# Kernel tuning notes

Hardware: AMD Instinct MI355X
Metric: run time of the kernel (lower is better)

## Reference

```python
import jax, jax.numpy as jnp
from jax import lax
import numpy as np


def _majority_filter(x, footprint_size, num_bins):
    # x: [B, H, W] float labels in [0, num_bins).
    # Faithful to torch majority_filter: replicate-pad, per-pixel histogram
    # (torch.histc bins=256 over [0,255] == integer-value counts for integer
    # labels; restricting to num_bins bins is exact since labels < num_bins),
    # mode = argmax of counts with ties broken toward the smaller label
    # (torch.argmax and jnp.argmax both return the first maximum).
    p = footprint_size // 2
    xp = jnp.pad(x, ((0, 0), (p, p), (p, p)), mode='edge')  # [B, H+2p, W+2p]
    bins = jnp.arange(num_bins, dtype=xp.dtype)
    onehot = (xp[..., None] == bins).astype(jnp.float32)  # [B, H+2p, W+2p, num_bins]
    counts = lax.reduce_window(
        onehot, jnp.float32(0), lax.add,
        window_dimensions=(1, footprint_size, footprint_size, 1),
        window_strides=(1, 1, 1, 1), padding='VALID')  # [B, H, W, num_bins]
    return jnp.argmax(counts, axis=-1).astype(x.dtype)


def setup_inputs() -> dict:
    key = jax.random.key(0)
    B, H, W = 8, 768, 768
    NUM_LABELS = 8  # cluster_range=(2, 8) -> labels in [0, 8)
    clusters = jax.random.randint(key, (B, H, W), 0, NUM_LABELS).astype(jnp.float32)
    return {"clusters": clusters, "footprint_size": 3, "num_bins": NUM_LABELS, "max_iter": 8}


def reference(clusters, footprint_size, num_bins, max_iter):
    # clean_clusters: iterate the majority filter up to max_iter times,
    # stopping early once the map is unchanged (|old - new| <= 1e-5 everywhere).
    def cond(state):
        t, i, changed = state
        return jnp.logical_and(i < max_iter, changed)

    def body(state):
        t, i, _ = state
        nt = _majority_filter(t, footprint_size, num_bins)
        changed = jnp.any(jnp.abs(t - nt) > 1e-5)
        return (nt, i + 1, changed)

    t, _, _ = lax.while_loop(cond, body, (clusters, jnp.int32(0), jnp.array(True)))
    return t
```

## Files before the change

### kernel.cpp

```cpp
#include <hip/hip_runtime.h>


static constexpr int IMG = 768;
static constexpr int NBX = 16;
static constexpr int NBY = 16;

__device__ __forceinline__ unsigned bfi(unsigned m, unsigned a, unsigned b) {
  unsigned r;
  asm("v_bfi_b32 %0, %1, %2, %3" : "=v"(r) : "v"(m), "v"(a), "v"(b));
  return r;
}
__device__ __forceinline__ unsigned dppUp(unsigned x) {
  return (unsigned)__builtin_amdgcn_update_dpp(0, (int)x, 0x138, 0xF, 0xF, true);
}
__device__ __forceinline__ unsigned dppDn(unsigned x) {
  return (unsigned)__builtin_amdgcn_update_dpp(0, (int)x, 0x130, 0xF, 0xF, true);
}
__device__ __forceinline__ unsigned alignb(unsigned hi, unsigned lo, int s) {
  return __builtin_amdgcn_alignbit(hi, lo, s);
}

struct C4 { unsigned b0, b1, b2, b3; };

__device__ __forceinline__ unsigned gt4(const C4& x, const C4& y) {
  unsigned d = x.b0 ^ y.b0;
  unsigned g = d & x.b0;
  d = x.b1 ^ y.b1; g = bfi(d, x.b1, g);
  d = x.b2 ^ y.b2; g = bfi(d, x.b2, g);
  d = x.b3 ^ y.b3; g = bfi(d, x.b3, g);
  return g;
}
__device__ __forceinline__ C4 sel4(unsigned G, const C4& x, const C4& y) {
  C4 r; r.b0 = bfi(G, x.b0, y.b0); r.b1 = bfi(G, x.b1, y.b1);
  r.b2 = bfi(G, x.b2, y.b2); r.b3 = bfi(G, x.b3, y.b3); return r;
}
__device__ __forceinline__ void tourn8(const C4 c[8],
                                       unsigned& o0, unsigned& o1, unsigned& o2) {
  unsigned g01 = gt4(c[1], c[0]); C4 w01 = sel4(g01, c[1], c[0]);
  unsigned g23 = gt4(c[3], c[2]); C4 w23 = sel4(g23, c[3], c[2]);
  unsigned gA  = gt4(w23, w01);   C4 wA  = sel4(gA, w23, w01);
  unsigned iA0 = bfi(gA, g23, g01), iA1 = gA;
  unsigned g45 = gt4(c[5], c[4]); C4 w45 = sel4(g45, c[5], c[4]);
  unsigned g67 = gt4(c[7], c[6]); C4 w67 = sel4(g67, c[7], c[6]);
  unsigned gB  = gt4(w67, w45);   C4 wB  = sel4(gB, w67, w45);
  unsigned iB0 = bfi(gB, g67, g45), iB1 = gB;
  unsigned gR  = gt4(wB, wA);
  o0 = bfi(gR, iB0, iA0); o1 = bfi(gR, iB1, iA1); o2 = gR;
}

__global__ __launch_bounds__(256, 2) void fused_dpp(
    const float* __restrict__ in, float* __restrict__ out) {
  const int wv = threadIdx.x >> 6;
  const int lane = threadIdx.x & 63;
  const int bx = blockIdx.x * 4 + wv;
  const int by = blockIdx.y, bz = blockIdx.z;

  const float* img = in + (size_t)bz * IMG * IMG;
  const int gyu = by * 48 - 8 + lane;

  unsigned p0l = 0, p1l = 0, p2l = 0, p0h = 0, p1h = 0, p2h = 0;
  {
    int gy = gyu < 0 ? 0 : (gyu > IMG - 1 ? IMG - 1 : gyu);
    const float* rp = img + (size_t)gy * IMG;
    const int gx0 = bx * 48 - 8;
    const int gxc = gx0 < 0 ? 0 : (gx0 > IMG - 64 ? IMG - 64 : gx0);
#pragma unroll
    for (int g = 0; g < 8; ++g) {
      float4 f = *reinterpret_cast<const float4*>(rp + gxc + 4 * g);
      unsigned u0 = (unsigned)(int)f.x, u1 = (unsigned)(int)f.y;
      unsigned u2 = (unsigned)(int)f.z, u3 = (unsigned)(int)f.w;
      p0l |= ((u0 & 1u) | ((u1 & 1u) << 1) | ((u2 & 1u) << 2) | ((u3 & 1u) << 3)) << (4 * g);
      p1l |= (((u0 >> 1) & 1u) | (((u1 >> 1) & 1u) << 1) | (((u2 >> 1) & 1u) << 2) | (((u3 >> 1) & 1u) << 3)) << (4 * g);
      p2l |= (((u0 >> 2) & 1u) | (((u1 >> 2) & 1u) << 1) | (((u2 >> 2) & 1u) << 2) | (((u3 >> 2) & 1u) << 3)) << (4 * g);
    }
#pragma unroll
    for (int g = 0; g < 8; ++g) {
      float4 f = *reinterpret_cast<const float4*>(rp + gxc + 32 + 4 * g);
      unsigned u0 = (unsigned)(int)f.x, u1 = (unsigned)(int)f.y;
      unsigned u2 = (unsigned)(int)f.z, u3 = (unsigned)(int)f.w;
      p0h |= ((u0 & 1u) | ((u1 & 1u) << 1) | ((u2 & 1u) << 2) | ((u3 & 1u) << 3)) << (4 * g);
      p1h |= (((u0 >> 1) & 1u) | (((u1 >> 1) & 1u) << 1) | (((u2 >> 1) & 1u) << 2) | (((u3 >> 1) & 1u) << 3)) << (4 * g);
      p2h |= (((u0 >> 2) & 1u) | (((u1 >> 2) & 1u) << 1) | (((u2 >> 2) & 1u) << 2) | (((u3 >> 2) & 1u) << 3)) << (4 * g);
    }
    if (bx == 0) {
      p0h = alignb(p0h, p0l, 24); p0l <<= 8;
      p1h = alignb(p1h, p1l, 24); p1l <<= 8;
      p2h = alignb(p2h, p2l, 24); p2l <<= 8;
    } else if (bx == NBX - 1) {
      p0l = alignb(p0h, p0l, 8); p0h >>= 8;
      p1l = alignb(p1h, p1l, 8); p1h >>= 8;
      p2l = alignb(p2h, p2l, 8); p2h >>= 8;
    }
  }

  const bool topE = (by == 0), botE = (by == NBY - 1);
  const bool lxE = (bx == 0), rxE = (bx == NBX - 1);
  const bool pTop = (lane == 8);
  const bool pBot = (lane == 55);

#pragma unroll 1
  for (int it = 0; it < 8; ++it) {
    unsigned e0[8], e1[8];
    {
      unsigned n0 = ~p0l, n1 = ~p1l, n2 = ~p2l;
      unsigned a00 = n1 & n0, a01 = n1 & p0l, a10 = p1l & n0, a11 = p1l & p0l;
      e0[0] = n2 & a00; e0[1] = n2 & a01; e0[2] = n2 & a10; e0[3] = n2 & a11;
      e0[4] = p2l & a00; e0[5] = p2l & a01; e0[6] = p2l & a10; e0[7] = p2l & a11;
    }
    {
      unsigned n0 = ~p0h, n1 = ~p1h, n2 = ~p2h;
      unsigned a00 = n1 & n0, a01 = n1 & p0h, a10 = p1h & n0, a11 = p1h & p0h;
      e1[0] = n2 & a00; e1[1] = n2 & a01; e1[2] = n2 & a10; e1[3] = n2 & a11;
      e1[4] = p2h & a00; e1[5] = p2h & a01; e1[6] = p2h & a10; e1[7] = p2h & a11;
    }

    unsigned euA[8], edA[8], euB[8], edB[8];
#pragma unroll
    for (int b = 0; b < 8; ++b) {
      euA[b] = dppUp(e0[b]); edA[b] = dppDn(e0[b]);
      euB[b] = dppUp(e1[b]); edB[b] = dppDn(e1[b]);
    }

    unsigned VL0[8], VH0[8], VL1[8], VH1[8];
#pragma unroll
    for (int b = 0; b < 8; ++b) {
      unsigned eu = euA[b], ed = edA[b];
      if (topE) eu = pTop ? e0[b] : eu;
      if (botE) ed = pBot ? e0[b] : ed;
      unsigned t = eu ^ e0[b];
      VL0[b] = t ^ ed; VH0[b] = bfi(t, ed, e0[b]);
      eu = euB[b]; ed = edB[b];
      if (topE) eu = pTop ? e1[b] : eu;
      if (botE) ed = pBot ? e1[b] : ed;
      t = eu ^ e1[b];
      VL1[b] = t ^ ed; VH1[b] = bfi(t, ed, e1[b]);
    }

    C4 c0[8], c1[8];
#pragma unroll
    for (int b = 0; b < 8; ++b) {
      unsigned AL0 = VL0[b] << 1,               AL1 = alignb(VL1[b], VL0[b], 31);
      unsigned AH0 = VH0[b] << 1,               AH1 = alignb(VH1[b], VH0[b], 31);
      unsigned CL0 = alignb(VL1[b], VL0[b], 1), CL1 = VL1[b] >> 1;
      unsigned CH0 = alignb(VH1[b], VH0[b], 1), CH1 = VH1[b] >> 1;
      if (lxE) { AL0 = bfi(0x100u, VL0[b], AL0); AH0 = bfi(0x100u, VH0[b], AH0); }
      if (rxE) { CL1 = bfi(0x00800000u, VL1[b], CL1); CH1 = bfi(0x00800000u, VH1[b], CH1); }

      unsigned s0 = AL0 ^ VL0[b], cc = AL0 & VL0[b];
      unsigned u  = AH0 ^ VH0[b];
      unsigned s1 = u ^ cc, s2 = bfi(u, cc, VH0[b]);
      unsigned t0 = s0 ^ CL0, k0 = s0 & CL0, vv = s1 ^ CH0;
      c0[b].b0 = t0; c0[b].b1 = vv ^ k0;
      unsigned k1 = bfi(vv, k0, CH0);
      c0[b].b2 = s2 ^ k1; c0[b].b3 = s2 & k1;
      s0 = AL1 ^ VL1[b]; cc = AL1 & VL1[b];
      u  = AH1 ^ VH1[b];
      s1 = u ^ cc; s2 = bfi(u, cc, VH1[b]);
      unsigned q0 = s0 ^ CL1; k0 = s0 & CL1; vv = s1 ^ CH1;
      c1[b].b0 = q0; c1[b].b1 = vv ^ k0;
      k1 = bfi(vv, k0, CH1);
      c1[b].b2 = s2 ^ k1; c1[b].b3 = s2 & k1;
    }

    tourn8(c0, p0l, p1l, p2l);
    tourn8(c1, p0h, p1h, p2h);
  }

  if (lane >= 8 && lane < 56) {
    float* orow = out + (size_t)bz * IMG * IMG + (size_t)gyu * IMG + bx * 48;
#pragma unroll
    for (int g = 0; g < 6; ++g) {
      const int j = 8 + 4 * g;
      float4 f;
      f.x = (float)(((p0l >> (j + 0)) & 1u) | (((p1l >> (j + 0)) & 1u) << 1) | (((p2l >> (j + 0)) & 1u) << 2));
      f.y = (float)(((p0l >> (j + 1)) & 1u) | (((p1l >> (j + 1)) & 1u) << 1) | (((p2l >> (j + 1)) & 1u) << 2));
      f.z = (float)(((p0l >> (j + 2)) & 1u) | (((p1l >> (j + 2)) & 1u) << 1) | (((p2l >> (j + 2)) & 1u) << 2));
      f.w = (float)(((p0l >> (j + 3)) & 1u) | (((p1l >> (j + 3)) & 1u) << 1) | (((p2l >> (j + 3)) & 1u) << 2));
      *reinterpret_cast<float4*>(orow + 4 * g) = f;
    }
#pragma unroll
    for (int g = 0; g < 6; ++g) {
      const int j = 4 * g;
      float4 f;
      f.x = (float)(((p0h >> (j + 0)) & 1u) | (((p1h >> (j + 0)) & 1u) << 1) | (((p2h >> (j + 0)) & 1u) << 2));
      f.y = (float)(((p0h >> (j + 1)) & 1u) | (((p1h >> (j + 1)) & 1u) << 1) | (((p2h >> (j + 1)) & 1u) << 2));
      f.z = (float)(((p0h >> (j + 2)) & 1u) | (((p1h >> (j + 2)) & 1u) << 1) | (((p2h >> (j + 2)) & 1u) << 2));
      f.w = (float)(((p0h >> (j + 3)) & 1u) | (((p1h >> (j + 3)) & 1u) << 1) | (((p2h >> (j + 3)) & 1u) << 2));
      *reinterpret_cast<float4*>(orow + 24 + 4 * g) = f;
    }
  }
}

extern "C" void kernel_launch(void* const* d_in, const int* in_sizes, int n_in,
                              void* d_out, int out_size, void* d_ws, size_t ws_size,
                              hipStream_t stream) {
  const float* clusters = (const float*)d_in[0];
  (void)in_sizes; (void)n_in; (void)out_size; (void)d_ws; (void)ws_size;

  dim3 grid(4, NBY, 8);
  fused_dpp<<<grid, 256, 0, stream>>>(clusters, (float*)d_out);
}
```

Baseline: 31.92 us.

## Split eight-iteration filter into two four-iteration kernels with smaller row halo

The single fused kernel that ran all eight majority-filter iterations with an 8-row halo is replaced by two kernels that each run four iterations. The first kernel stores the bit-packed label planes to a workspace, and the second reloads them. Needing only a 4-row halo raises the useful rows per wave from 48 to 56 and shrinks the grid from 16 to 14 row tiles, cutting redundant halo computation. In exchange it adds a second launch, a dependency between the kernels and a workspace write/read round trip, and 448 blocks no longer fill the GPU as evenly as 512 did.

```diff
diff --git a/kernel.cpp b/kernel.cpp
--- a/kernel.cpp
+++ b/kernel.cpp
@@ -3,7 +3,7 @@
 
 static constexpr int IMG = 768;
 static constexpr int NBX = 16;
-static constexpr int NBY = 16;
+static constexpr int NYT = 14;
 
 __device__ __forceinline__ unsigned bfi(unsigned m, unsigned a, unsigned b) {
   unsigned r;
@@ -48,58 +48,12 @@
   o0 = bfi(gR, iB0, iA0); o1 = bfi(gR, iB1, iA1); o2 = gR;
 }
 
-__global__ __launch_bounds__(256, 2) void fused_dpp(
-    const float* __restrict__ in, float* __restrict__ out) {
-  const int wv = threadIdx.x >> 6;
-  const int lane = threadIdx.x & 63;
-  const int bx = blockIdx.x * 4 + wv;
-  const int by = blockIdx.y, bz = blockIdx.z;
-
-  const float* img = in + (size_t)bz * IMG * IMG;
-  const int gyu = by * 48 - 8 + lane;
-
-  unsigned p0l = 0, p1l = 0, p2l = 0, p0h = 0, p1h = 0, p2h = 0;
-  {
-    int gy = gyu < 0 ? 0 : (gyu > IMG - 1 ? IMG - 1 : gyu);
-    const float* rp = img + (size_t)gy * IMG;
-    const int gx0 = bx * 48 - 8;
-    const int gxc = gx0 < 0 ? 0 : (gx0 > IMG - 64 ? IMG - 64 : gx0);
-#pragma unroll
-    for (int g = 0; g < 8; ++g) {
-      float4 f = *reinterpret_cast<const float4*>(rp + gxc + 4 * g);
-      unsigned u0 = (unsigned)(int)f.x, u1 = (unsigned)(int)f.y;
-      unsigned u2 = (unsigned)(int)f.z, u3 = (unsigned)(int)f.w;
-      p0l |= ((u0 & 1u) | ((u1 & 1u) << 1) | ((u2 & 1u) << 2) | ((u3 & 1u) << 3)) << (4 * g);
-      p1l |= (((u0 >> 1) & 1u) | (((u1 >> 1) & 1u) << 1) | (((u2 >> 1) & 1u) << 2) | (((u3 >> 1) & 1u) << 3)) << (4 * g);
-      p2l |= (((u0 >> 2) & 1u) | (((u1 >> 2) & 1u) << 1) | (((u2 >> 2) & 1u) << 2) | (((u3 >> 2) & 1u) << 3)) << (4 * g);
-    }
-#pragma unroll
-    for (int g = 0; g < 8; ++g) {
-      float4 f = *reinterpret_cast<const float4*>(rp + gxc + 32 + 4 * g);
-      unsigned u0 = (unsigned)(int)f.x, u1 = (unsigned)(int)f.y;
-      unsigned u2 = (unsigned)(int)f.z, u3 = (unsigned)(int)f.w;
-      p0h |= ((u0 & 1u) | ((u1 & 1u) << 1) | ((u2 & 1u) << 2) | ((u3 & 1u) << 3)) << (4 * g);
-      p1h |= (((u0 >> 1) & 1u) | (((u1 >> 1) & 1u) << 1) | (((u2 >> 1) & 1u) << 2) | (((u3 >> 1) & 1u) << 3)) << (4 * g);
-      p2h |= (((u0 >> 2) & 1u) | (((u1 >> 2) & 1u) << 1) | (((u2 >> 2) & 1u) << 2) | (((u3 >> 2) & 1u) << 3)) << (4 * g);
-    }
-    if (bx == 0) {
-      p0h = alignb(p0h, p0l, 24); p0l <<= 8;
-      p1h = alignb(p1h, p1l, 24); p1l <<= 8;
-      p2h = alignb(p2h, p2l, 24); p2l <<= 8;
-    } else if (bx == NBX - 1) {
-      p0l = alignb(p0h, p0l, 8); p0h >>= 8;
-      p1l = alignb(p1h, p1l, 8); p1h >>= 8;
-      p2l = alignb(p2h, p2l, 8); p2h >>= 8;
-    }
-  }
-
-  const bool topE = (by == 0), botE = (by == NBY - 1);
-  const bool lxE = (bx == 0), rxE = (bx == NBX - 1);
-  const bool pTop = (lane == 8);
-  const bool pBot = (lane == 55);
-
+__device__ __forceinline__ void iter4(
+    unsigned& p0l, unsigned& p1l, unsigned& p2l,
+    unsigned& p0h, unsigned& p1h, unsigned& p2h,
+    bool topE, bool botE, bool lxE, bool rxE, bool pTop, bool pBot) {
 #pragma unroll 1
-  for (int it = 0; it < 8; ++it) {
+  for (int it = 0; it < 4; ++it) {
     unsigned e0[8], e1[8];
     {
       unsigned n0 = ~p0l, n1 = ~p1l, n2 = ~p2l;
@@ -165,8 +119,89 @@
     tourn8(c0, p0l, p1l, p2l);
     tourn8(c1, p0h, p1h, p2h);
   }
-
-  if (lane >= 8 && lane < 56) {
+}
+
+__device__ __forceinline__ size_t wsIdx(int b, int p, int w, int xt, int row) {
+  return (size_t)((((b * 3 + p) * 2 + w) * 16 + xt)) * IMG + row;
+}
+
+__global__ __launch_bounds__(256, 2) void phaseA(
+    const float* __restrict__ in, unsigned* __restrict__ ws) {
+  const int wv = threadIdx.x >> 6, lane = threadIdx.x & 63;
+  const int bx = blockIdx.x * 4 + wv;
+  const int by = blockIdx.y, bz = blockIdx.z;
+  const float* img = in + (size_t)bz * IMG * IMG;
+  const int gyu = by * 56 - 4 + lane;
+
+  unsigned p0l = 0, p1l = 0, p2l = 0, p0h = 0, p1h = 0, p2h = 0;
+  {
+    int gy = gyu < 0 ? 0 : (gyu > IMG - 1 ? IMG - 1 : gyu);
+    const float* rp = img + (size_t)gy * IMG;
+    const int gx0 = bx * 48 - 8;
+    const int gxc = gx0 < 0 ? 0 : (gx0 > IMG - 64 ? IMG - 64 : gx0);
+#pragma unroll
+    for (int g = 0; g < 8; ++g) {
+      float4 f = *reinterpret_cast<const float4*>(rp + gxc + 4 * g);
+      unsigned u0 = (unsigned)(int)f.x, u1 = (unsigned)(int)f.y;
+      unsigned u2 = (unsigned)(int)f.z, u3 = (unsigned)(int)f.w;
+      p0l |= ((u0 & 1u) | ((u1 & 1u) << 1) | ((u2 & 1u) << 2) | ((u3 & 1u) << 3)) << (4 * g);
+      p1l |= (((u0 >> 1) & 1u) | (((u1 >> 1) & 1u) << 1) | (((u2 >> 1) & 1u) << 2) | (((u3 >> 1) & 1u) << 3)) << (4 * g);
+      p2l |= (((u0 >> 2) & 1u) | (((u1 >> 2) & 1u) << 1) | (((u2 >> 2) & 1u) << 2) | (((u3 >> 2) & 1u) << 3)) << (4 * g);
+    }
+#pragma unroll
+    for (int g = 0; g < 8; ++g) {
+      float4 f = *reinterpret_cast<const float4*>(rp + gxc + 32 + 4 * g);
+      unsigned u0 = (unsigned)(int)f.x, u1 = (unsigned)(int)f.y;
+      unsigned u2 = (unsigned)(int)f.z, u3 = (unsigned)(int)f.w;
+      p0h |= ((u0 & 1u) | ((u1 & 1u) << 1) | ((u2 & 1u) << 2) | ((u3 & 1u) << 3)) << (4 * g);
+      p1h |= (((u0 >> 1) & 1u) | (((u1 >> 1) & 1u) << 1) | (((u2 >> 1) & 1u) << 2) | (((u3 >> 1) & 1u) << 3)) << (4 * g);
+      p2h |= (((u0 >> 2) & 1u) | (((u1 >> 2) & 1u) << 1) | (((u2 >> 2) & 1u) << 2) | (((u3 >> 2) & 1u) << 3)) << (4 * g);
+    }
+    if (bx == 0) {
+      p0h = alignb(p0h, p0l, 24); p0l <<= 8;
+      p1h = alignb(p1h, p1l, 24); p1l <<= 8;
+      p2h = alignb(p2h, p2l, 24); p2l <<= 8;
+    } else if (bx == NBX - 1) {
+      p0l = alignb(p0h, p0l, 8); p0h >>= 8;
+      p1l = alignb(p1h, p1l, 8); p1h >>= 8;
+      p2l = alignb(p2h, p2l, 8); p2h >>= 8;
+    }
+  }
+
+  iter4(p0l, p1l, p2l, p0h, p1h, p2h,
+        by == 0, by == NYT - 1, bx == 0, bx == NBX - 1,
+        gyu == 0, gyu == IMG - 1);
+
+  if (lane >= 4 && lane < 60 && gyu < IMG) {
+    ws[wsIdx(bz, 0, 0, bx, gyu)] = p0l;
+    ws[wsIdx(bz, 0, 1, bx, gyu)] = p0h;
+    ws[wsIdx(bz, 1, 0, bx, gyu)] = p1l;
+    ws[wsIdx(bz, 1, 1, bx, gyu)] = p1h;
+    ws[wsIdx(bz, 2, 0, bx, gyu)] = p2l;
+    ws[wsIdx(bz, 2, 1, bx, gyu)] = p2h;
+  }
+}
+
+__global__ __launch_bounds__(256, 2) void phaseB(
+    const unsigned* __restrict__ ws, float* __restrict__ out) {
+  const int wv = threadIdx.x >> 6, lane = threadIdx.x & 63;
+  const int bx = blockIdx.x * 4 + wv;
+  const int by = blockIdx.y, bz = blockIdx.z;
+  const int gyu = by * 56 - 4 + lane;
+  const int gy = gyu < 0 ? 0 : (gyu > IMG - 1 ? IMG - 1 : gyu);
+
+  unsigned p0l = ws[wsIdx(bz, 0, 0, bx, gy)];
+  unsigned p0h = ws[wsIdx(bz, 0, 1, bx, gy)];
+  unsigned p1l = ws[wsIdx(bz, 1, 0, bx, gy)];
+  unsigned p1h = ws[wsIdx(bz, 1, 1, bx, gy)];
+  unsigned p2l = ws[wsIdx(bz, 2, 0, bx, gy)];
+  unsigned p2h = ws[wsIdx(bz, 2, 1, bx, gy)];
+
+  iter4(p0l, p1l, p2l, p0h, p1h, p2h,
+        by == 0, by == NYT - 1, bx == 0, bx == NBX - 1,
+        gyu == 0, gyu == IMG - 1);
+
+  if (lane >= 4 && lane < 60 && gyu < IMG) {
     float* orow = out + (size_t)bz * IMG * IMG + (size_t)gyu * IMG + bx * 48;
 #pragma unroll
     for (int g = 0; g < 6; ++g) {
@@ -195,8 +230,9 @@
                               void* d_out, int out_size, void* d_ws, size_t ws_size,
                               hipStream_t stream) {
   const float* clusters = (const float*)d_in[0];
-  (void)in_sizes; (void)n_in; (void)out_size; (void)d_ws; (void)ws_size;
-
-  dim3 grid(4, NBY, 8);
-  fused_dpp<<<grid, 256, 0, stream>>>(clusters, (float*)d_out);
-}
+  (void)in_sizes; (void)n_in; (void)out_size; (void)ws_size;
+
+  dim3 grid(4, NYT, 8);
+  phaseA<<<grid, 256, 0, stream>>>(clusters, (unsigned*)d_ws);
+  phaseB<<<grid, 256, 0, stream>>>((const unsigned*)d_ws, (float*)d_out);
+}
```

Result: slower. 37.67 us (+18.0%).
